# Optimization experiments

Hardware: AMD Instinct MI355X
Metric: run time of the kernel (lower is better)

Reference implementation:

```python
import jax, jax.numpy as jnp
import numpy as np

CHNN = 1024
K = 2048


def _conv1x1(W, b, x):
    # x: (B, C_in, L), W: (C_out, C_in), b: (C_out,)
    return jnp.einsum('oc,bcl->bol', W, x) + b[None, :, None]


def setup_inputs() -> dict:
    key = jax.random.key(0)
    ks = jax.random.split(key, 10)
    s = 0.02
    return {
        'vc': jax.random.normal(ks[0], (1, CHNN, K), dtype=jnp.float32),
        'vm': jax.random.normal(ks[1], (1, CHNN, K), dtype=jnp.float32),
        'W_ak': jax.random.normal(ks[2], (K, CHNN), dtype=jnp.float32) * s,
        'b_ak': jax.random.normal(ks[3], (K,), dtype=jnp.float32) * s,
        'W_c': jax.random.normal(ks[4], (CHNN, CHNN), dtype=jnp.float32) * s,
        'b_c': jax.random.normal(ks[5], (CHNN,), dtype=jnp.float32) * s,
        'W_mad': jax.random.normal(ks[6], (CHNN, CHNN), dtype=jnp.float32) * s,
        'b_mad': jax.random.normal(ks[7], (CHNN,), dtype=jnp.float32) * s,
        'W_gcn': jax.random.normal(ks[8], (CHNN, CHNN), dtype=jnp.float32) * s,
        'b_gcn': jax.random.normal(ks[9], (CHNN,), dtype=jnp.float32) * s,
    }


def reference(vc, vm, W_ak, b_ak, W_c, b_c, W_mad, b_mad, W_gcn, b_gcn):
    # vcw: (1, K, L) assignment logits; softmax over the K (channel) dim
    vcw = _conv1x1(W_ak, b_ak, vc)
    vcw = jax.nn.softmax(vcw, axis=1)
    w = vcw[0].T                      # (L, K)  (batch forced to 1 by squeeze(0))
    # vm features: (1, CHNN, K)
    vmr = jax.nn.relu(_conv1x1(W_c, b_c, vm))
    # F.linear(vm, w): contract last dim (K) with w's second dim -> (1, CHNN, L)
    vma = jnp.einsum('bck,lk->bcl', vmr, w)
    vma = _conv1x1(W_mad, b_mad, vma)  # (1, CHNN, L)
    # dense adjacency over positions: (1, L, L)
    A = jnp.einsum('bck,bcl->bkl', vma, vma)
    # GCN: x (1, K, CHNN) @ W + b, then softmax(A) @ x  (requires L == K)
    x = jnp.swapaxes(vmr, 1, 2) @ W_gcn + b_gcn
    A = jax.nn.softmax(A, axis=-1)
    out = A @ x                        # (1, L, CHNN)
    return jnp.swapaxes(out, 1, 2)     # (1, CHNN, L)
```

## Files before the change

### kernel.cpp

```cpp
#include <hip/hip_runtime.h>
#include <hip/hip_bf16.h>


typedef __bf16 bf16x4 __attribute__((ext_vector_type(4)));
typedef __bf16 bf16x8 __attribute__((ext_vector_type(8)));
typedef float  f32x4  __attribute__((ext_vector_type(4)));

typedef const void __attribute__((address_space(1)))* gptr_t;
typedef void       __attribute__((address_space(3)))* lptr_t;

__device__ __forceinline__ void load16_lds(const __bf16* g, __bf16* l)
{
    __builtin_amdgcn_global_load_lds((gptr_t)g, (lptr_t)l, 16, 0, 0);
}

template<typename OT, int TM_, int TN_, int BIAS_, bool RELU_, int STORE_>
struct GC {
    using OUT_T = OT;
    static constexpr int TM = TM_, TN = TN_, BIAS = BIAS_, STORE = STORE_;
    static constexpr bool RELU = RELU_;
    static constexpr int SMEM = 2 * (TM_ + TN_) * 32 * 2;
};

template<class CF>
__device__ __forceinline__ void gemm_body(
    int bid, char* smem,
    const __bf16* __restrict__ A, const __bf16* __restrict__ B,
    const float* __restrict__ bias,
    typename CF::OUT_T* __restrict__ C, typename CF::OUT_T* __restrict__ CT,
    int M, int N, int K, int ntx)
{
    constexpr int TM = CF::TM, TN = CF::TN;
    constexpr int FM = TM / 32, FN = TN / 32;
    constexpr int NA = TM / 64, NB = TN / 64;
    __bf16* sA = (__bf16*)smem;
    __bf16* sB = (__bf16*)smem + 2 * TM * 32;
    const int tid = threadIdx.x, lane = tid & 63, wv = tid >> 6;
    const int m0 = (bid / ntx) * TM, n0 = (bid % ntx) * TN;
    const int mw = (wv >> 1) * (FM * 16), nw = (wv & 1) * (FN * 16);

    f32x4 acc[FM][FN];
    #pragma unroll
    for (int i = 0; i < FM; ++i)
        #pragma unroll
        for (int j = 0; j < FN; ++j)
            acc[i][j] = (f32x4){0.f, 0.f, 0.f, 0.f};

    const __bf16* gA = A + (size_t)m0 * K;
    const __bf16* gB = B + (size_t)n0 * K;

    auto stage = [&](int k0, int buf) {
        #pragma unroll
        for (int i = 0; i < NA; ++i) {
            const int c = (wv * NA + i) * 64 + lane;
            load16_lds(gA + (size_t)(c >> 2) * K + k0 + (c & 3) * 8,
                       &sA[buf * TM * 32 + (wv * NA + i) * 512]);
        }
        #pragma unroll
        for (int i = 0; i < NB; ++i) {
            const int c = (wv * NB + i) * 64 + lane;
            load16_lds(gB + (size_t)(c >> 2) * K + k0 + (c & 3) * 8,
                       &sB[buf * TN * 32 + (wv * NB + i) * 512]);
        }
    };

    stage(0, 0);
    int cur = 0;
    for (int k0 = 0; k0 < K; k0 += 32) {
        __syncthreads();
        if (k0 + 32 < K) stage(k0 + 32, cur ^ 1);
        bf16x8 af[FM], bfr[FN];
        #pragma unroll
        for (int i = 0; i < FM; ++i)
            af[i] = *(const bf16x8*)&sA[cur * TM * 32 + (mw + i * 16 + (lane & 15)) * 32 + (lane >> 4) * 8];
        #pragma unroll
        for (int j = 0; j < FN; ++j)
            bfr[j] = *(const bf16x8*)&sB[cur * TN * 32 + (nw + j * 16 + (lane & 15)) * 32 + (lane >> 4) * 8];
        #pragma unroll
        for (int i = 0; i < FM; ++i)
            #pragma unroll
            for (int j = 0; j < FN; ++j)
                acc[i][j] = __builtin_amdgcn_mfma_f32_16x16x32_bf16(af[i], bfr[j], acc[i][j], 0, 0, 0);
        cur ^= 1;
    }

    #pragma unroll
    for (int i = 0; i < FM; ++i) {
        const int rowb = m0 + mw + i * 16 + (lane >> 4) * 4;
        #pragma unroll
        for (int j = 0; j < FN; ++j) {
            const int col = n0 + nw + j * 16 + (lane & 15);
            f32x4 v = acc[i][j];
            #pragma unroll
            for (int r = 0; r < 4; ++r) {
                float f = v[r];
                if (CF::BIAS == 1) f += bias[rowb + r];
                if (CF::BIAS == 2) f += bias[col];
                if (CF::RELU) f = fmaxf(f, 0.f);
                v[r] = f;
            }
            if (CF::STORE == 0 || CF::STORE == 2) {
                #pragma unroll
                for (int r = 0; r < 4; ++r)
                    C[(size_t)(rowb + r) * N + col] = (typename CF::OUT_T)v[r];
            }
            if (CF::STORE == 1 || CF::STORE == 2) {
                if constexpr (sizeof(typename CF::OUT_T) == 4) {
                    *(f32x4*)&CT[(size_t)col * M + rowb] = v;
                } else {
                    bf16x4 w = { (__bf16)v[0], (__bf16)v[1], (__bf16)v[2], (__bf16)v[3] };
                    *(bf16x4*)&CT[(size_t)col * M + rowb] = w;
                }
            }
        }
    }
}

template<class CF>
__global__ __launch_bounds__(256, 2)
void gemm1(const __bf16* __restrict__ A, const __bf16* __restrict__ B,
           const float* __restrict__ bias,
           typename CF::OUT_T* __restrict__ C, typename CF::OUT_T* __restrict__ CT,
           int M, int N, int K, int ntx)
{
    __shared__ char smem[CF::SMEM];
    gemm_body<CF>(blockIdx.x, smem, A, B, bias, C, CT, M, N, K, ntx);
}

template<class C1, class C2>
__global__ __launch_bounds__(256, 2)
void gemm2(int nblk1,
           const __bf16* __restrict__ A1, const __bf16* __restrict__ B1,
           const float* __restrict__ b1,
           typename C1::OUT_T* __restrict__ C1p, typename C1::OUT_T* __restrict__ CT1,
           int M1, int N1, int K1, int ntx1,
           const __bf16* __restrict__ A2, const __bf16* __restrict__ B2,
           const float* __restrict__ b2,
           typename C2::OUT_T* __restrict__ C2p, typename C2::OUT_T* __restrict__ CT2,
           int M2, int N2, int K2, int ntx2)
{
    constexpr int S = C1::SMEM > C2::SMEM ? C1::SMEM : C2::SMEM;
    __shared__ char smem[S];
    if ((int)blockIdx.x < nblk1)
        gemm_body<C1>(blockIdx.x, smem, A1, B1, b1, C1p, CT1, M1, N1, K1, ntx1);
    else
        gemm_body<C2>(blockIdx.x - nblk1, smem, A2, B2, b2, C2p, CT2, M2, N2, K2, ntx2);
}

__device__ __forceinline__ void tp_tile(const float* __restrict__ in,
                                        __bf16* __restrict__ outp,
                                        int R, int C, int bx, int by)
{
    __shared__ float t[32][33];
    const int tx = threadIdx.x & 31, ty = threadIdx.x >> 5;
    #pragma unroll
    for (int i = ty; i < 32; i += 8)
        t[i][tx] = in[(size_t)(by + i) * C + (bx + tx)];
    __syncthreads();
    #pragma unroll
    for (int i = ty; i < 32; i += 8)
        outp[(size_t)(bx + i) * R + (by + tx)] = (__bf16)t[tx][i];
}

__device__ __forceinline__ void cast_blk(const float* __restrict__ s,
                                         __bf16* __restrict__ d, int blk)
{
    const int i = blk * 1024 + threadIdx.x * 4;
    float4 v = *(const float4*)&s[i];
    bf16x4 w = { (__bf16)v.x, (__bf16)v.y, (__bf16)v.z, (__bf16)v.w };
    *(bf16x4*)&d[i] = w;
}

__device__ __forceinline__ void softmax_row(__bf16* __restrict__ p)
{
    __shared__ float red[256];
    const int t = threadIdx.x;
    bf16x8 v = *(bf16x8*)&p[t * 8];
    float f[8];
    float m = -1e30f;
    #pragma unroll
    for (int r = 0; r < 8; ++r) { f[r] = (float)v[r]; m = fmaxf(m, f[r]); }
    red[t] = m;
    __syncthreads();
    for (int s = 128; s > 0; s >>= 1) {
        if (t < s) red[t] = fmaxf(red[t], red[t + s]);
        __syncthreads();
    }
    m = red[0];
    __syncthreads();
    float sum = 0.f;
    #pragma unroll
    for (int r = 0; r < 8; ++r) { f[r] = expf(f[r] - m); sum += f[r]; }
    red[t] = sum;
    __syncthreads();
    for (int s = 128; s > 0; s >>= 1) {
        if (t < s) red[t] += red[t + s];
        __syncthreads();
    }
    const float inv = 1.f / red[0];
    bf16x8 w;
    #pragma unroll
    for (int r = 0; r < 8; ++r) w[r] = (__bf16)(f[r] * inv);
    *(bf16x8*)&p[t * 8] = w;
}

__global__ __launch_bounds__(256)
void prep(const float* __restrict__ vc, __bf16* __restrict__ vcT,
          const float* __restrict__ vm, __bf16* __restrict__ vmT,
          const float* __restrict__ W_ak, __bf16* __restrict__ W_akb,
          const float* __restrict__ W_c, __bf16* __restrict__ W_cb)
{
    if (blockIdx.z == 0) {
        int e = blockIdx.x;
        const float* in  = (e < 2048) ? vc : vcT ? (e < 2048 ? vc : vm) : vm;
        in = (e < 2048) ? vc : vm;
        __bf16* o = (e < 2048) ? vcT : vmT;
        e &= 2047;
        tp_tile(in, o, 1024, 2048, (e & 63) * 32, (e >> 6) * 32);
    } else {
        const int x = blockIdx.x;
        if (x >= 3072) return;
        if (x < 2048) cast_blk(W_ak, W_akb, x);
        else          cast_blk(W_c, W_cb, x - 2048);
    }
}

__global__ __launch_bounds__(256)
void smprep(__bf16* __restrict__ ST,
            const float* __restrict__ W_mad, __bf16* __restrict__ W_madb,
            const float* __restrict__ W_gcn, __bf16* __restrict__ W_gcnT)
{
    if (blockIdx.z == 0) {
        softmax_row(ST + (size_t)blockIdx.x * 2048);
    } else if (blockIdx.z == 1) {
        if (blockIdx.x >= 1024) return;
        cast_blk(W_mad, W_madb, blockIdx.x);
    } else {
        if (blockIdx.x >= 1024) return;
        const int e = blockIdx.x;
        tp_tile(W_gcn, W_gcnT, 1024, 1024, (e & 31) * 32, (e >> 5) * 32);
    }
}

__global__ __launch_bounds__(256)
void row_softmax_k(__bf16* __restrict__ A)
{
    softmax_row(A + (size_t)blockIdx.x * 2048);
}

extern "C" void kernel_launch(void* const* d_in, const int* in_sizes, int n_in,
                              void* d_out, int out_size, void* d_ws, size_t ws_size,
                              hipStream_t stream)
{
    const float* vc    = (const float*)d_in[0];
    const float* vm    = (const float*)d_in[1];
    const float* W_ak  = (const float*)d_in[2];
    const float* b_ak  = (const float*)d_in[3];
    const float* W_c   = (const float*)d_in[4];
    const float* b_c   = (const float*)d_in[5];
    const float* W_mad = (const float*)d_in[6];
    const float* b_mad = (const float*)d_in[7];
    const float* W_gcn = (const float*)d_in[8];
    const float* b_gcn = (const float*)d_in[9];
    float* out = (float*)d_out;

    char* ws = (char*)d_ws;
    const size_t MB = 1u << 20;
    __bf16* ST     = (__bf16*)(ws);
    __bf16* P      = (__bf16*)(ws);
    __bf16* vcT    = (__bf16*)(ws + 8 * MB);
    __bf16* vma1T  = (__bf16*)(ws + 8 * MB);
    __bf16* W_akb  = (__bf16*)(ws + 12 * MB);
    __bf16* vmaT   = (__bf16*)(ws + 12 * MB);
    __bf16* vmT    = (__bf16*)(ws + 16 * MB);
    __bf16* xT     = (__bf16*)(ws + 16 * MB);
    __bf16* W_cb   = (__bf16*)(ws + 20 * MB);
    __bf16* W_madb = (__bf16*)(ws + 20 * MB);
    __bf16* W_gcnT = (__bf16*)(ws + 22 * MB);
    __bf16* vmr    = (__bf16*)(ws + 24 * MB);
    __bf16* vmrT   = (__bf16*)(ws + 28 * MB);

    using G3  = GC<__bf16, 128, 128, 2, false, 0>;
    using G5  = GC<__bf16, 128, 128, 1, true,  2>;
    using G7  = GC<__bf16, 128, 128, 0, false, 0>;
    using G11 = GC<__bf16, 128, 128, 1, false, 0>;
    using G8  = GC<__bf16, 128, 64,  2, false, 0>;
    using G9  = GC<__bf16, 128, 128, 0, false, 0>;
    using G12 = GC<float,  128, 64,  0, false, 1>;

    prep<<<dim3(4096, 1, 2), 256, 0, stream>>>(vc, vcT, vm, vmT, W_ak, W_akb, W_c, W_cb);
    gemm2<G3, G5><<<384, 256, 0, stream>>>(256,
        vcT, W_akb, b_ak, ST, (__bf16*)nullptr, 2048, 2048, 1024, 16,
        W_cb, vmT, b_c, vmr, vmrT, 1024, 2048, 1024, 16);
    smprep<<<dim3(2048, 1, 3), 256, 0, stream>>>(ST, W_mad, W_madb, W_gcn, W_gcnT);
    gemm2<G7, G11><<<256, 256, 0, stream>>>(128,
        ST, vmr, nullptr, vma1T, (__bf16*)nullptr, 2048, 1024, 2048, 8,
        W_gcnT, vmrT, b_gcn, xT, (__bf16*)nullptr, 1024, 2048, 1024, 16);
    gemm1<G8><<<256, 256, 0, stream>>>(vma1T, W_madb, b_mad, vmaT, (__bf16*)nullptr,
                                       2048, 1024, 1024, 16);
    gemm1<G9><<<256, 256, 0, stream>>>(vmaT, vmaT, nullptr, P, (__bf16*)nullptr,
                                       2048, 2048, 1024, 16);
    row_softmax_k<<<2048, 256, 0, stream>>>(P);
    gemm1<G12><<<256, 256, 0, stream>>>(P, xT, nullptr, (float*)nullptr, out,
                                        2048, 1024, 2048, 16);
}
```

Measured before the change: 223.4 us.

## Shrink GEMM tiles to fill more CUs and regroup weight prep into one kernel

Halves the GEMM output tiles (128x128 to 128x64, and 128x64 to 64x64) and doubles the grid sizes, so every GEMM launch puts more workgroups across the CUs. The W_mad cast and W_gcn transpose move from the old smprep kernel into the first prep kernel. The first softmax now runs in the existing row_softmax kernel. The transposed W_gcn is staged in the output buffer, which is overwritten later, to free workspace. Smaller tiles trade less operand reuse per workgroup and more global/LDS traffic for better load balance.

```diff
diff --git a/kernel.cpp b/kernel.cpp
--- a/kernel.cpp
+++ b/kernel.cpp
@@ -208,37 +208,23 @@
 void prep(const float* __restrict__ vc, __bf16* __restrict__ vcT,
           const float* __restrict__ vm, __bf16* __restrict__ vmT,
           const float* __restrict__ W_ak, __bf16* __restrict__ W_akb,
-          const float* __restrict__ W_c, __bf16* __restrict__ W_cb)
-{
+          const float* __restrict__ W_c, __bf16* __restrict__ W_cb,
+          const float* __restrict__ W_mad, __bf16* __restrict__ W_madb,
+          const float* __restrict__ W_gcn, __bf16* __restrict__ W_gcnT)
+{
+    const int x = blockIdx.x;
     if (blockIdx.z == 0) {
-        int e = blockIdx.x;
-        const float* in  = (e < 2048) ? vc : vcT ? (e < 2048 ? vc : vm) : vm;
-        in = (e < 2048) ? vc : vm;
-        __bf16* o = (e < 2048) ? vcT : vmT;
-        e &= 2047;
+        const float* in = (x < 2048) ? vc : vm;
+        __bf16* o       = (x < 2048) ? vcT : vmT;
+        const int e = x & 2047;
         tp_tile(in, o, 1024, 2048, (e & 63) * 32, (e >> 6) * 32);
+    } else if (blockIdx.z == 1) {
+        if (x < 2048)      cast_blk(W_ak, W_akb, x);
+        else if (x < 3072) cast_blk(W_c, W_cb, x - 2048);
+        else               cast_blk(W_mad, W_madb, x - 3072);
     } else {
-        const int x = blockIdx.x;
-        if (x >= 3072) return;
-        if (x < 2048) cast_blk(W_ak, W_akb, x);
-        else          cast_blk(W_c, W_cb, x - 2048);
-    }
-}
-
-__global__ __launch_bounds__(256)
-void smprep(__bf16* __restrict__ ST,
-            const float* __restrict__ W_mad, __bf16* __restrict__ W_madb,
-            const float* __restrict__ W_gcn, __bf16* __restrict__ W_gcnT)
-{
-    if (blockIdx.z == 0) {
-        softmax_row(ST + (size_t)blockIdx.x * 2048);
-    } else if (blockIdx.z == 1) {
-        if (blockIdx.x >= 1024) return;
-        cast_blk(W_mad, W_madb, blockIdx.x);
-    } else {
-        if (blockIdx.x >= 1024) return;
-        const int e = blockIdx.x;
-        tp_tile(W_gcn, W_gcnT, 1024, 1024, (e & 31) * 32, (e >> 5) * 32);
+        if (x >= 1024) return;
+        tp_tile(W_gcn, W_gcnT, 1024, 1024, (x & 31) * 32, (x >> 5) * 32);
     }
 }
 
@@ -275,32 +261,35 @@
     __bf16* vmT    = (__bf16*)(ws + 16 * MB);
     __bf16* xT     = (__bf16*)(ws + 16 * MB);
     __bf16* W_cb   = (__bf16*)(ws + 20 * MB);
-    __bf16* W_madb = (__bf16*)(ws + 20 * MB);
-    __bf16* W_gcnT = (__bf16*)(ws + 22 * MB);
+    __bf16* W_madb = (__bf16*)(ws + 22 * MB);
     __bf16* vmr    = (__bf16*)(ws + 24 * MB);
     __bf16* vmrT   = (__bf16*)(ws + 28 * MB);
-
-    using G3  = GC<__bf16, 128, 128, 2, false, 0>;
-    using G5  = GC<__bf16, 128, 128, 1, true,  2>;
-    using G7  = GC<__bf16, 128, 128, 0, false, 0>;
-    using G11 = GC<__bf16, 128, 128, 1, false, 0>;
-    using G8  = GC<__bf16, 128, 64,  2, false, 0>;
-    using G9  = GC<__bf16, 128, 128, 0, false, 0>;
-    using G12 = GC<float,  128, 64,  0, false, 1>;
-
-    prep<<<dim3(4096, 1, 2), 256, 0, stream>>>(vc, vcT, vm, vmT, W_ak, W_akb, W_c, W_cb);
-    gemm2<G3, G5><<<384, 256, 0, stream>>>(256,
-        vcT, W_akb, b_ak, ST, (__bf16*)nullptr, 2048, 2048, 1024, 16,
-        W_cb, vmT, b_c, vmr, vmrT, 1024, 2048, 1024, 16);
-    smprep<<<dim3(2048, 1, 3), 256, 0, stream>>>(ST, W_mad, W_madb, W_gcn, W_gcnT);
-    gemm2<G7, G11><<<256, 256, 0, stream>>>(128,
-        ST, vmr, nullptr, vma1T, (__bf16*)nullptr, 2048, 1024, 2048, 8,
-        W_gcnT, vmrT, b_gcn, xT, (__bf16*)nullptr, 1024, 2048, 1024, 16);
-    gemm1<G8><<<256, 256, 0, stream>>>(vma1T, W_madb, b_mad, vmaT, (__bf16*)nullptr,
+    __bf16* W_gcnT = (__bf16*)(ws + 20 * MB);
+    W_gcnT = (__bf16*)((char*)d_out + 0);
+
+    using G3  = GC<__bf16, 128, 64, 2, false, 0>;
+    using G5  = GC<__bf16, 128, 64, 1, true,  2>;
+    using G7  = GC<__bf16, 128, 64, 0, false, 0>;
+    using G11 = GC<__bf16, 128, 64, 1, false, 0>;
+    using G8  = GC<__bf16, 64,  64, 2, false, 0>;
+    using G9  = GC<__bf16, 128, 64, 0, false, 0>;
+    using G12 = GC<float,  64,  64, 0, false, 1>;
+
+    prep<<<dim3(4096, 1, 3), 256, 0, stream>>>(vc, vcT, vm, vmT, W_ak, W_akb,
+                                               W_c, W_cb, W_mad, W_madb,
+                                               W_gcn, W_gcnT);
+    gemm2<G3, G5><<<768, 256, 0, stream>>>(512,
+        vcT, W_akb, b_ak, ST, (__bf16*)nullptr, 2048, 2048, 1024, 32,
+        W_cb, vmT, b_c, vmr, vmrT, 1024, 2048, 1024, 32);
+    row_softmax_k<<<2048, 256, 0, stream>>>(ST);
+    gemm2<G7, G11><<<512, 256, 0, stream>>>(256,
+        ST, vmr, nullptr, vma1T, (__bf16*)nullptr, 2048, 1024, 2048, 16,
+        W_gcnT, vmrT, b_gcn, xT, (__bf16*)nullptr, 1024, 2048, 1024, 32);
+    gemm1<G8><<<512, 256, 0, stream>>>(vma1T, W_madb, b_mad, vmaT, (__bf16*)nullptr,
                                        2048, 1024, 1024, 16);
-    gemm1<G9><<<256, 256, 0, stream>>>(vmaT, vmaT, nullptr, P, (__bf16*)nullptr,
-                                       2048, 2048, 1024, 16);
+    gemm1<G9><<<512, 256, 0, stream>>>(vmaT, vmaT, nullptr, P, (__bf16*)nullptr,
+                                       2048, 2048, 1024, 32);
     row_softmax_k<<<2048, 256, 0, stream>>>(P);
-    gemm1<G12><<<256, 256, 0, stream>>>(P, xT, nullptr, (float*)nullptr, out,
+    gemm1<G12><<<512, 256, 0, stream>>>(P, xT, nullptr, (float*)nullptr, out,
                                         2048, 1024, 2048, 16);
 }
```

New measurement: 214.6 us. -3.9%, faster.
